# Kernel tuning notes

Measured on AMD Instinct MI355X. Metric: run time of the kernel, lower is better.

The kernel has to match this reference:

```python
import jax, jax.numpy as jnp
import numpy as np

D_MODEL, STATE_DIM = 256, 16
BATCH, SEQLEN = 8, 2048


def setup_inputs() -> dict:
    key = jax.random.key(0)
    k1, k2, k3, k4, k5 = jax.random.split(key, 5)
    x = jax.random.normal(k1, (BATCH, SEQLEN, D_MODEL), dtype=jnp.float32)
    # A is parameterized as -exp(randn) in the torch module's init
    A = -jnp.exp(jax.random.normal(k2, (D_MODEL, STATE_DIM), dtype=jnp.float32))
    B = jax.random.normal(k3, (D_MODEL, STATE_DIM), dtype=jnp.float32)
    C = jax.random.normal(k4, (D_MODEL, STATE_DIM), dtype=jnp.float32)
    D = jnp.ones((D_MODEL,), dtype=jnp.float32)
    delta = jax.random.uniform(k5, (D_MODEL,), dtype=jnp.float32) * 0.1 + 0.001
    return {"x": x, "A": A, "B": B, "C": C, "D": D, "delta": delta}


def reference(x, A, B, C, D, delta):
    # x: (Bsz, L, D_model); A,B,C: (D_model, N); D,delta: (D_model,)
    dt = jax.nn.sigmoid(delta)[:, None]          # (D, 1)
    A_bar = jnp.exp(dt * A)                      # (D, N), time-invariant
    B_bar = dt * B                               # (D, N)

    def step(h, x_t):
        # h: (Bsz, D, N); x_t: (Bsz, D)
        h = A_bar[None] * h + B_bar[None] * x_t[:, :, None]
        y_t = jnp.einsum('bdn,dn->bd', h, C)
        return h, y_t

    h0 = jnp.zeros((x.shape[0], x.shape[2], A.shape[1]), dtype=x.dtype)
    _, ys = jax.lax.scan(step, h0, jnp.swapaxes(x, 0, 1))  # ys: (L, Bsz, D)
    y = jnp.swapaxes(ys, 0, 1)                   # (Bsz, L, D)
    return y + x * D[None, None, :]
```

## Files before the change

### kernel.cpp

```cpp
#include <hip/hip_runtime.h>

#define BSZ  8
#define LSEQ 2048
#define DM   256
#define NS   16
#define NC   32
#define LC   (LSEQ/NC)
#define TILE_FLOATS (LC * DM)
#define VEC_ROUNDS  (TILE_FLOATS / 4 / DM)

__global__ void k_local(
        const float* __restrict__ x,
        const float* __restrict__ A,
        const float* __restrict__ Bm,
        const float* __restrict__ delta,
        float* __restrict__ carry) {
    __shared__ float lx[TILE_FLOATS];
    const int d     = threadIdx.x;
    const int chunk = blockIdx.x & (NC - 1);
    const int b     = blockIdx.x / NC;

    {
        const float4* __restrict__ src =
            (const float4*)(x + ((size_t)(b * LSEQ + chunk * LC)) * DM);
        float4* dst = (float4*)lx;
#pragma unroll
        for (int r = 0; r < VEC_ROUNDS; ++r)
            dst[r * DM + d] = src[r * DM + d];
    }

    const float dt = 1.0f / (1.0f + expf(-delta[d]));
    float a[NS], bb[NS];
#pragma unroll
    for (int n = 0; n < NS; ++n) {
        a[n]  = expf(dt * A[d * NS + n]);
        bb[n] = dt * Bm[d * NS + n];
    }
    __syncthreads();

    float h[NS];
#pragma unroll
    for (int n = 0; n < NS; ++n) h[n] = 0.0f;
#pragma unroll 4
    for (int t = 0; t < LC; ++t) {
        const float xv = lx[t * DM + d];
#pragma unroll
        for (int n = 0; n < NS; ++n) h[n] = fmaf(a[n], h[n], bb[n] * xv);
    }

    float* cp = carry + ((size_t)(b * NC + chunk) * NS) * DM + d;
#pragma unroll
    for (int n = 0; n < NS; ++n) cp[(size_t)n * DM] = h[n];
}

__global__ void k_prefix(
        const float* __restrict__ A,
        const float* __restrict__ delta,
        float* __restrict__ carry) {
    const int tid = blockIdx.x * 256 + threadIdx.x;
    const int d = tid & (DM - 1);
    const int n = (tid >> 8) & (NS - 1);
    const int b = tid >> 12;

    const float dt = 1.0f / (1.0f + expf(-delta[d]));
    const float aL = expf(dt * A[d * NS + n] * (float)LC);

    float run = 0.0f;
    float* cp = carry + (size_t)b * NC * NS * DM + (size_t)n * DM + d;
#pragma unroll
    for (int j = 0; j < NC; ++j) {
        const size_t off = (size_t)j * NS * DM;
        const float c = cp[off];
        cp[off] = run;
        run = fmaf(aL, run, c);
    }
}

__global__ void k_final(
        const float* __restrict__ x,
        const float* __restrict__ A,
        const float* __restrict__ Bm,
        const float* __restrict__ Cm,
        const float* __restrict__ Dv,
        const float* __restrict__ delta,
        const float* __restrict__ hin,
        float* __restrict__ y) {
    __shared__ float lt[TILE_FLOATS];
    const int d     = threadIdx.x;
    const int chunk = blockIdx.x & (NC - 1);
    const int b     = blockIdx.x / NC;

    const size_t tile_base = ((size_t)(b * LSEQ + chunk * LC)) * DM;
    {
        const float4* __restrict__ src = (const float4*)(x + tile_base);
        float4* dst = (float4*)lt;
#pragma unroll
        for (int r = 0; r < VEC_ROUNDS; ++r)
            dst[r * DM + d] = src[r * DM + d];
    }

    const float dt = 1.0f / (1.0f + expf(-delta[d]));
    float a[NS], bb[NS], cc[NS];
#pragma unroll
    for (int n = 0; n < NS; ++n) {
        a[n]  = expf(dt * A[d * NS + n]);
        bb[n] = dt * Bm[d * NS + n];
        cc[n] = Cm[d * NS + n];
    }
    const float Dd = Dv[d];

    float h[NS];
    const float* hp = hin + ((size_t)(b * NC + chunk) * NS) * DM + d;
#pragma unroll
    for (int n = 0; n < NS; ++n) h[n] = hp[(size_t)n * DM];

    __syncthreads();

#pragma unroll 4
    for (int t = 0; t < LC; ++t) {
        const float xv = lt[t * DM + d];
        float acc = Dd * xv;
#pragma unroll
        for (int n = 0; n < NS; ++n) {
            h[n] = fmaf(a[n], h[n], bb[n] * xv);
            acc  = fmaf(h[n], cc[n], acc);
        }
        lt[t * DM + d] = acc;
    }
    __syncthreads();

    {
        float4* __restrict__ dst = (float4*)(y + tile_base);
        const float4* src = (const float4*)lt;
#pragma unroll
        for (int r = 0; r < VEC_ROUNDS; ++r)
            dst[r * DM + d] = src[r * DM + d];
    }
}

extern "C" void kernel_launch(void* const* d_in, const int* in_sizes, int n_in,
                              void* d_out, int out_size, void* d_ws, size_t ws_size,
                              hipStream_t stream) {
    const float* x     = (const float*)d_in[0];
    const float* A     = (const float*)d_in[1];
    const float* Bm    = (const float*)d_in[2];
    const float* Cm    = (const float*)d_in[3];
    const float* Dv    = (const float*)d_in[4];
    const float* delta = (const float*)d_in[5];
    float* y = (float*)d_out;

    float* carry = (float*)d_ws;

    dim3 blk(DM);
    dim3 grd1(BSZ * NC);
    k_local<<<grd1, blk, 0, stream>>>(x, A, Bm, delta, carry);

    dim3 grd2((BSZ * NS * DM) / 256);
    k_prefix<<<grd2, dim3(256), 0, stream>>>(A, delta, carry);

    k_final<<<grd1, blk, 0, stream>>>(x, A, Bm, Cm, Dv, delta, carry, y);
}
```

Baseline: 28.59 us.

## Fold carry prefix scan into final kernel, drop separate prefix launch

New measurement: 35.01 us. 22.5% more time.

```diff
diff --git a/kernel.cpp b/kernel.cpp
--- a/kernel.cpp
+++ b/kernel.cpp
@@ -53,29 +53,6 @@
     for (int n = 0; n < NS; ++n) cp[(size_t)n * DM] = h[n];
 }
 
-__global__ void k_prefix(
-        const float* __restrict__ A,
-        const float* __restrict__ delta,
-        float* __restrict__ carry) {
-    const int tid = blockIdx.x * 256 + threadIdx.x;
-    const int d = tid & (DM - 1);
-    const int n = (tid >> 8) & (NS - 1);
-    const int b = tid >> 12;
-
-    const float dt = 1.0f / (1.0f + expf(-delta[d]));
-    const float aL = expf(dt * A[d * NS + n] * (float)LC);
-
-    float run = 0.0f;
-    float* cp = carry + (size_t)b * NC * NS * DM + (size_t)n * DM + d;
-#pragma unroll
-    for (int j = 0; j < NC; ++j) {
-        const size_t off = (size_t)j * NS * DM;
-        const float c = cp[off];
-        cp[off] = run;
-        run = fmaf(aL, run, c);
-    }
-}
-
 __global__ void k_final(
         const float* __restrict__ x,
         const float* __restrict__ A,
@@ -83,7 +60,7 @@
         const float* __restrict__ Cm,
         const float* __restrict__ Dv,
         const float* __restrict__ delta,
-        const float* __restrict__ hin,
+        const float* __restrict__ carry,
         float* __restrict__ y) {
     __shared__ float lt[TILE_FLOATS];
     const int d     = threadIdx.x;
@@ -100,20 +77,30 @@
     }
 
     const float dt = 1.0f / (1.0f + expf(-delta[d]));
-    float a[NS], bb[NS], cc[NS];
+    float a[NS], bb[NS], cc[NS], aL[NS];
 #pragma unroll
     for (int n = 0; n < NS; ++n) {
-        a[n]  = expf(dt * A[d * NS + n]);
+        const float An = A[d * NS + n];
+        a[n]  = expf(dt * An);
+        aL[n] = expf(dt * An * (float)LC);
         bb[n] = dt * Bm[d * NS + n];
         cc[n] = Cm[d * NS + n];
     }
     const float Dd = Dv[d];
 
     float h[NS];
-    const float* hp = hin + ((size_t)(b * NC + chunk) * NS) * DM + d;
 #pragma unroll
-    for (int n = 0; n < NS; ++n) h[n] = hp[(size_t)n * DM];
-
+    for (int n = 0; n < NS; ++n) h[n] = 0.0f;
+    {
+        const float* cb = carry + ((size_t)b * NC * NS) * DM + d;
+#pragma unroll 2
+        for (int i = 0; i < chunk; ++i) {
+            const float* ci = cb + (size_t)i * NS * DM;
+#pragma unroll
+            for (int n = 0; n < NS; ++n)
+                h[n] = fmaf(aL[n], h[n], ci[(size_t)n * DM]);
+        }
+    }
     __syncthreads();
 
 #pragma unroll 4
@@ -128,7 +115,6 @@
         lt[t * DM + d] = acc;
     }
     __syncthreads();
-
     {
         float4* __restrict__ dst = (float4*)(y + tile_base);
         const float4* src = (const float4*)lt;
@@ -152,11 +138,7 @@
     float* carry = (float*)d_ws;
 
     dim3 blk(DM);
-    dim3 grd1(BSZ * NC);
-    k_local<<<grd1, blk, 0, stream>>>(x, A, Bm, delta, carry);
-
-    dim3 grd2((BSZ * NS * DM) / 256);
-    k_prefix<<<grd2, dim3(256), 0, stream>>>(A, delta, carry);
-
-    k_final<<<grd1, blk, 0, stream>>>(x, A, Bm, Cm, Dv, delta, carry, y);
+    dim3 grd(BSZ * NC);
+    k_local<<<grd, blk, 0, stream>>>(x, A, Bm, delta, carry);
+    k_final<<<grd, blk, 0, stream>>>(x, A, Bm, Cm, Dv, delta, carry, y);
 }
```
